# Performance work log

Measured on AMD Instinct MI355X. Metric: run time of the kernel, lower is better.

The kernel has to match this reference:

```python
import jax, jax.numpy as jnp
import numpy as np

N_HEAD = 16

def rel_shift(x):
    # x: (qlen, klen, B, n). Pad one zero column at front of klen axis,
    # reinterpret as (klen+1, qlen, B, n), drop first row, reshape back.
    qlen, klen, b, n = x.shape
    x_pad = jnp.pad(x, ((0, 0), (1, 0), (0, 0), (0, 0)))
    x_pad = x_pad.reshape(klen + 1, qlen, b, n)
    return x_pad[1:].reshape(qlen, klen, b, n)

def setup_inputs() -> dict:
    key = jax.random.key(0)
    ks = jax.random.split(key, 9)
    qlen = klen = 1024
    B = 4
    d_model = 1024
    d_head = d_model // N_HEAD
    q = jax.random.normal(ks[0], (qlen, B, d_model), jnp.float32)
    K = jax.random.normal(ks[1], (klen, B, d_model), jnp.float32)
    V = jax.random.normal(ks[2], (klen, B, d_model), jnp.float32)
    mask = jax.random.bernoulli(ks[3], 0.1, (1, klen, B, 1))
    r = jax.random.normal(ks[4], (klen, d_model), jnp.float32)
    u = jax.random.normal(ks[5], (N_HEAD, d_head), jnp.float32) * 0.02
    v = jax.random.normal(ks[6], (N_HEAD, d_head), jnp.float32) * 0.02
    Wr = jax.random.normal(ks[7], (d_model, d_model), jnp.float32) / np.sqrt(d_model)
    br = jax.random.normal(ks[8], (d_model,), jnp.float32) * 0.02
    return {"q": q, "K": K, "V": V, "mask": mask, "r": r, "u": u, "v": v, "Wr": Wr, "br": br}

def reference(q, K, V, mask, r, u, v, Wr, br):
    qlen, bsz, d_model = q.shape
    klen = K.shape[0]
    d_head = d_model // N_HEAD
    qh = q.reshape(qlen, bsz, N_HEAD, d_head)
    Kh = K.reshape(klen, bsz, N_HEAD, d_head)
    Vh = V.reshape(klen, bsz, N_HEAD, d_head)
    rh = (r @ Wr.T + br).reshape(klen, N_HEAD, d_head)  # r_net projection
    AC = jnp.einsum('ibnd,jbnd->ijbn', qh + u, Kh)
    BD = rel_shift(jnp.einsum('ibnd,jnd->ijbn', qh + v, rh))
    score = (AC + BD) / jnp.sqrt(jnp.asarray(d_head, q.dtype))
    # mask (1,klen,B,1) broadcasts over qlen and heads (torch repeats over heads)
    score = jnp.where(mask, jnp.asarray(-1e9, score.dtype), score)
    weight = jax.nn.softmax(score, axis=1)
    out = jnp.einsum('ijbn,jbnd->ibnd', weight, Vh).reshape(qlen, bsz, d_model)
    return out, weight.mean(axis=-1)
```

## Files before the change

### kernel.cpp

```cpp
#include <hip/hip_runtime.h>
#include <hip/hip_fp16.h>
#include <stdint.h>


#define L 1024
#define BATCH 4
#define NH 16
#define DH 64
#define DM 1024
#define TI 16
#define NJT 16
#define BDP_ST 1032
#define SCALE 0.125f
#define CS 0.18033688011112042f

typedef __attribute__((ext_vector_type(8))) short short8;
typedef __attribute__((ext_vector_type(4))) float f32x4;

static __device__ __forceinline__ unsigned short f2bf(float f) {
    union { float f; unsigned int u; } x; x.f = f;
    return (unsigned short)((x.u + 0x7fffu + ((x.u >> 16) & 1u)) >> 16);
}
static __device__ __forceinline__ float bf2f(unsigned short h) {
    union { unsigned int u; float f; } x; x.u = ((unsigned int)h) << 16;
    return x.f;
}
static __device__ __forceinline__ unsigned short f2h(float f) {
    __half h = __float2half(f);
    union { __half h; unsigned short s; } x; x.h = h; return x.s;
}
static __device__ __forceinline__ float h2f(unsigned short s) {
    union { __half h; unsigned short s; } x; x.s = s; return __half2float(x.h);
}
static __device__ __forceinline__ unsigned short* usp(void* base, int byteoff) {
    return (unsigned short*)((char*)base + byteoff);
}
static __device__ __forceinline__ short8 ld8(const void* base, int byteoff) {
    return *(const short8*)((const char*)base + byteoff);
}
static __device__ __forceinline__ float fexp2(float x) {
#if __has_builtin(__builtin_amdgcn_exp2f)
    return __builtin_amdgcn_exp2f(x);
#else
    return __expf(x * 0.6931471805599453f);
#endif
}
#define SW128(row, colByte) ((((row) * 128) + (colByte)) ^ (((row) & 7) << 4))

__global__ __launch_bounds__(256) void rh_gemm_mfma(
    const float* __restrict__ r, const float* __restrict__ Wr,
    const float* __restrict__ br, unsigned short* __restrict__ rhb)
{
    __shared__ unsigned short rT[64 * 64];
    __shared__ unsigned short wT[64 * 64];
    const int c0 = blockIdx.x * 64, m0 = blockIdx.y * 64;
    const int tid = threadIdx.x;
    const int w = tid >> 6, lane = tid & 63, lr = lane & 15, lg = lane >> 4;
    f32x4 acc[4] = {};

    for (int kt = 0; kt < 16; ++kt) {
        const int k0 = kt * 64;
        __syncthreads();
        const int row = tid >> 2, cb = (tid & 3) * 16;
#pragma unroll
        for (int q4 = 0; q4 < 4; ++q4) {
            float4 rv = *(const float4*)(r + (size_t)(c0 + row) * DM + k0 + cb + q4 * 4);
            unsigned short* p = usp(rT, SW128(row, (cb + q4 * 4) * 2));
            p[0] = f2bf(rv.x); p[1] = f2bf(rv.y); p[2] = f2bf(rv.z); p[3] = f2bf(rv.w);
            float4 wv = *(const float4*)(Wr + (size_t)(m0 + row) * DM + k0 + cb + q4 * 4);
            unsigned short* pw = usp(wT, SW128(row, (cb + q4 * 4) * 2));
            pw[0] = f2bf(wv.x); pw[1] = f2bf(wv.y); pw[2] = f2bf(wv.z); pw[3] = f2bf(wv.w);
        }
        __syncthreads();
#pragma unroll
        for (int mch = 0; mch < 4; ++mch)
#pragma unroll
            for (int kh = 0; kh < 2; ++kh) {
                short8 a  = ld8(rT, SW128(w * 16 + lr,   (kh * 32 + lg * 8) * 2));
                short8 bb = ld8(wT, SW128(mch * 16 + lr, (kh * 32 + lg * 8) * 2));
                acc[mch] = __builtin_amdgcn_mfma_f32_16x16x32_bf16(a, bb, acc[mch], 0, 0, 0);
            }
    }
#pragma unroll
    for (int mch = 0; mch < 4; ++mch)
#pragma unroll
        for (int r2 = 0; r2 < 4; ++r2) {
            const int c = c0 + w * 16 + lg * 4 + r2;
            const int d = mch * 16 + lr;
            const float val = acc[mch][r2] + br[m0 + d];
            rhb[((size_t)blockIdx.y * L + c) * DH + d] = f2bf(val);
        }
}

__global__ __launch_bounds__(256) void rh_gemm_kernel(
    const float* __restrict__ r, const float* __restrict__ Wr,
    const float* __restrict__ br, float* __restrict__ rhf)
{
    __shared__ float As[16][65];
    __shared__ float Bs[16][65];
    const int j0 = blockIdx.x * 64;
    const int m0 = blockIdx.y * 64;
    const int tid = threadIdx.x;
    const int ty = tid >> 4, tx = tid & 15;
    float acc[4][4] = {};

    for (int k0 = 0; k0 < DM; k0 += 16) {
        const int row = tid >> 2, c4 = (tid & 3) << 2;
        float4 av = *(const float4*)(r  + (size_t)(j0 + row) * DM + k0 + c4);
        float4 bv = *(const float4*)(Wr + (size_t)(m0 + row) * DM + k0 + c4);
        __syncthreads();
        As[c4 + 0][row] = av.x; As[c4 + 1][row] = av.y;
        As[c4 + 2][row] = av.z; As[c4 + 3][row] = av.w;
        Bs[c4 + 0][row] = bv.x; Bs[c4 + 1][row] = bv.y;
        Bs[c4 + 2][row] = bv.z; Bs[c4 + 3][row] = bv.w;
        __syncthreads();
#pragma unroll
        for (int k = 0; k < 16; ++k) {
            float a[4], bb[4];
#pragma unroll
            for (int t = 0; t < 4; ++t) { a[t] = As[k][ty * 4 + t]; bb[t] = Bs[k][tx * 4 + t]; }
#pragma unroll
            for (int ii = 0; ii < 4; ++ii)
#pragma unroll
                for (int jj = 0; jj < 4; ++jj)
                    acc[ii][jj] = fmaf(a[ii], bb[jj], acc[ii][jj]);
        }
    }
#pragma unroll
    for (int ii = 0; ii < 4; ++ii) {
        const int row = j0 + ty * 4 + ii;
#pragma unroll
        for (int jj = 0; jj < 4; ++jj) {
            const int col = m0 + tx * 4 + jj;
            rhf[(size_t)row * DM + col] = acc[ii][jj] + br[col];
        }
    }
}

__global__ __launch_bounds__(256) void prepass_kernel(
    const float* __restrict__ Kg, const float* __restrict__ Vg,
    unsigned short* __restrict__ Kbf, unsigned short* __restrict__ Vtb)
{
    __shared__ unsigned short tile[64][80];
    const int j0 = blockIdx.x * 64;
    const int b = blockIdx.y, n = blockIdx.z;
    const int bn = b * NH + n;
    const int tid = threadIdx.x;

    for (int idx = tid; idx < 64 * 16; idx += 256) {
        const int jr = idx >> 4, s4 = (idx & 15) * 4;
        const size_t src = ((size_t)(j0 + jr) * BATCH + b) * DM + n * DH + s4;
        float4 kv = *(const float4*)(Kg + src);
        ushort4 o;
        o.x = f2bf(kv.x); o.y = f2bf(kv.y); o.z = f2bf(kv.z); o.w = f2bf(kv.w);
        *(ushort4*)(Kbf + ((size_t)bn * L + j0 + jr) * DH + s4) = o;
        float4 vv4 = *(const float4*)(Vg + src);
        tile[s4 + 0][jr] = f2bf(vv4.x); tile[s4 + 1][jr] = f2bf(vv4.y);
        tile[s4 + 2][jr] = f2bf(vv4.z); tile[s4 + 3][jr] = f2bf(vv4.w);
    }
    __syncthreads();
    for (int idx = tid; idx < 64 * 8; idx += 256) {
        const int d = idx >> 3, p8 = (idx & 7) * 8;
        short8 o = *(const short8*)&tile[d][p8];
        *(short8*)(Vtb + ((size_t)bn * DH + d) * L + j0 + p8) = o;
    }
}

__global__ __launch_bounds__(256) void wm_reduce_kernel(
    const unsigned short* __restrict__ W_ws, const float* __restrict__ rdeng,
    float* __restrict__ wm_out)
{
    const int gi = blockIdx.x;
    const int b  = blockIdx.y;
    const int j0 = threadIdx.x * 4;
    float a0 = 0.f, a1 = 0.f, a2 = 0.f, a3 = 0.f;
#pragma unroll
    for (int n = 0; n < NH; ++n) {
        const int bn = b * NH + n;
        const float rd = rdeng[((size_t)bn << 10) + gi];
        ushort4 wv = *(const ushort4*)(W_ws + ((size_t)bn * L + gi) * L + j0);
        a0 += bf2f(wv.x) * rd; a1 += bf2f(wv.y) * rd;
        a2 += bf2f(wv.z) * rd; a3 += bf2f(wv.w) * rd;
    }
    const size_t o = ((size_t)gi * L + j0) * BATCH + b;
    wm_out[o]             = a0;
    wm_out[o + BATCH]     = a1;
    wm_out[o + 2 * BATCH] = a2;
    wm_out[o + 3 * BATCH] = a3;
}

__global__ __launch_bounds__(256, 3) void attn_fused(
    const float* __restrict__ q,
    const unsigned short* __restrict__ Kbf, const unsigned short* __restrict__ Vtb,
    const unsigned char* __restrict__ maskp,
    const float* __restrict__ uu, const float* __restrict__ vvp,
    const unsigned short* __restrict__ rhb,
    float* __restrict__ out, unsigned short* __restrict__ W_ws,
    float* __restrict__ rdeng)
{
    __shared__ __align__(16) unsigned short BDp[17 * BDP_ST];
    __shared__ __align__(16) unsigned short Wt[4][2][16 * 64];
    __shared__ unsigned char mblk[L];
    __shared__ float denomP[4][16];
    __shared__ float rdenom[16];
    __shared__ int mflags;

    const int i0 = blockIdx.x * TI;
    const int b  = blockIdx.y;
    const int n  = blockIdx.z;
    const int bn = b * NH + n;
    const int tid = threadIdx.x;
    const int w = tid >> 6, lane = tid & 63, lr = lane & 15, lg = lane >> 4;

    if (tid == 0) mflags = 0;
    __syncthreads();
    {
        int local = 0;
        for (int ww = tid; ww < 1024; ww += 256) {
            const unsigned int word = ((const unsigned int*)maskp)[ww];
            if (word == 0x3f800000u) local |= 1;
            else if (word & 0xffffff00u) local |= 2;
        }
        if (local) atomicOr(&mflags, local);
    }
    __syncthreads();
    {
        const int mtype = (mflags & 1) ? 2 : ((mflags & 2) ? 1 : 0);
        for (int j = tid; j < L; j += 256) {
            bool mv;
            if (mtype == 2)      mv = ((const float*)maskp)[j * BATCH + b] != 0.f;
            else if (mtype == 1) mv = maskp[j * BATCH + b] != 0;
            else                 mv = ((const int*)maskp)[j * BATCH + b] != 0;
            mblk[j] = mv ? 1 : 0;
        }
    }
    if (tid < 17 * 8) {
        const int row = tid >> 3, cp = tid & 7;
        BDp[row * BDP_ST + 1024 + cp] = 0;
    }

    const float* qrow = q + ((size_t)(i0 + lr) * BATCH + b) * DM + n * DH;
    const float* urow = uu + n * DH;
    const float* vrow = vvp + n * DH;
    short8 qu_a[2], qv_a[2];
#pragma unroll
    for (int kh = 0; kh < 2; ++kh) {
        const int kb = kh * 32 + lg * 8;
        float4 qa = *(const float4*)(qrow + kb), qb = *(const float4*)(qrow + kb + 4);
        float4 ua = *(const float4*)(urow + kb), ub = *(const float4*)(urow + kb + 4);
        float4 va = *(const float4*)(vrow + kb), vb = *(const float4*)(vrow + kb + 4);
        short8 su, sv;
        su[0] = (short)f2bf((qa.x + ua.x) * CS); su[1] = (short)f2bf((qa.y + ua.y) * CS);
        su[2] = (short)f2bf((qa.z + ua.z) * CS); su[3] = (short)f2bf((qa.w + ua.w) * CS);
        su[4] = (short)f2bf((qb.x + ub.x) * CS); su[5] = (short)f2bf((qb.y + ub.y) * CS);
        su[6] = (short)f2bf((qb.z + ub.z) * CS); su[7] = (short)f2bf((qb.w + ub.w) * CS);
        sv[0] = (short)f2bf((qa.x + va.x) * CS); sv[1] = (short)f2bf((qa.y + va.y) * CS);
        sv[2] = (short)f2bf((qa.z + va.z) * CS); sv[3] = (short)f2bf((qa.w + va.w) * CS);
        sv[4] = (short)f2bf((qb.x + vb.x) * CS); sv[5] = (short)f2bf((qb.y + vb.y) * CS);
        sv[6] = (short)f2bf((qb.z + vb.z) * CS); sv[7] = (short)f2bf((qb.w + vb.w) * CS);
        qu_a[kh] = su; qv_a[kh] = sv;
    }
    float qv16[16];
    {
        const int kq = (tid & 3) * 16;
        if (i0 + 16 < L) {
            const float* q16 = q + ((size_t)(i0 + 16) * BATCH + b) * DM + n * DH;
#pragma unroll
            for (int e4 = 0; e4 < 4; ++e4) {
                float4 qa = *(const float4*)(q16 + kq + e4 * 4);
                float4 va = *(const float4*)(vrow + kq + e4 * 4);
                qv16[e4 * 4 + 0] = (qa.x + va.x) * CS; qv16[e4 * 4 + 1] = (qa.y + va.y) * CS;
                qv16[e4 * 4 + 2] = (qa.z + va.z) * CS; qv16[e4 * 4 + 3] = (qa.w + va.w) * CS;
            }
        } else {
#pragma unroll
            for (int e = 0; e < 16; ++e) qv16[e] = 0.f;
        }
    }

    {
        const unsigned short* rpane = rhb + (size_t)n * L * DH;
        const int ccol = w * 16 + lr;
        short8 rb[2][2];
#pragma unroll
        for (int kh = 0; kh < 2; ++kh)
            rb[0][kh] = *(const short8*)(rpane + (size_t)ccol * DH + kh * 32 + lg * 8);
        const int col16 = tid >> 2;
        const int kq = (tid & 3) * 16;
#pragma unroll
        for (int ct = 0; ct < 16; ++ct) {
            const int c0 = ct * 64;
            const int cur = ct & 1;
            if (ct + 1 < 16) {
#pragma unroll
                for (int kh = 0; kh < 2; ++kh)
                    rb[cur ^ 1][kh] = *(const short8*)(rpane + (size_t)((ct + 1) * 64 + ccol) * DH + kh * 32 + lg * 8);
            }
            f32x4 acc = {0.f, 0.f, 0.f, 0.f};
#pragma unroll
            for (int kh = 0; kh < 2; ++kh)
                acc = __builtin_amdgcn_mfma_f32_16x16x32_bf16(qv_a[kh], rb[cur][kh], acc, 0, 0, 0);
#pragma unroll
            for (int r2 = 0; r2 < 4; ++r2)
                BDp[(lg * 4 + r2) * BDP_ST + c0 + ccol] = f2h(acc[r2]);
            {
                short8 ra0 = *(const short8*)(rpane + (size_t)(c0 + col16) * DH + kq);
                short8 ra1 = *(const short8*)(rpane + (size_t)(c0 + col16) * DH + kq + 8);
                float s16 = 0.f;
#pragma unroll
                for (int e = 0; e < 8; ++e) {
                    s16 = fmaf(qv16[e],     bf2f((unsigned short)ra0[e]), s16);
                    s16 = fmaf(qv16[e + 8], bf2f((unsigned short)ra1[e]), s16);
                }
                s16 += __shfl_xor(s16, 1);
                s16 += __shfl_xor(s16, 2);
                if ((tid & 3) == 0) BDp[16 * BDP_ST + c0 + col16] = f2h(s16);
            }
        }
    }
    __syncthreads();

    const unsigned short* Kpane = Kbf + (size_t)bn * L * DH;
    const unsigned short* Vpane = Vtb + (size_t)bn * DH * L;
    const int jwbase = w * 256;
    f32x4 pv[4] = {};
    float dl[4] = {0.f, 0.f, 0.f, 0.f};
    int ilb[4];
    size_t wsrow[4];
#pragma unroll
    for (int r2 = 0; r2 < 4; ++r2) {
        ilb[r2] = (lg * 4 + r2) * BDP_ST;
        wsrow[r2] = ((size_t)bn * L + i0 + lg * 4 + r2) * L;
    }
    short8 kf[2][2];
#pragma unroll
    for (int kh = 0; kh < 2; ++kh)
        kf[0][kh] = *(const short8*)(Kpane + (size_t)(jwbase + lr) * DH + kh * 32 + lg * 8);

#pragma unroll 1
    for (int sub = 0; sub < 4; ++sub) {
        const int jbase = jwbase + sub * 64;
        unsigned short* WtW = &Wt[w][sub & 1][0];
        short8 vfr[8];
#pragma unroll
        for (int dch = 0; dch < 4; ++dch)
#pragma unroll
            for (int kh = 0; kh < 2; ++kh)
                vfr[dch * 2 + kh] = *(const short8*)(Vpane + (size_t)(dch * 16 + lr) * L + jbase + kh * 32 + lg * 8);
#pragma unroll
        for (int c4 = 0; c4 < 4; ++c4) {
            const int chunk = sub * 4 + c4;
            const int cur = c4 & 1;
            if (chunk + 1 < 16) {
#pragma unroll
                for (int kh = 0; kh < 2; ++kh)
                    kf[cur ^ 1][kh] = *(const short8*)(Kpane + (size_t)(jwbase + (chunk + 1) * 16 + lr) * DH + kh * 32 + lg * 8);
            }
            f32x4 acc = {0.f, 0.f, 0.f, 0.f};
#pragma unroll
            for (int kh = 0; kh < 2; ++kh)
                acc = __builtin_amdgcn_mfma_f32_16x16x32_bf16(qu_a[kh], kf[cur][kh], acc, 0, 0, 0);
            const int gj = jbase + c4 * 16 + lr;
            const float mo = mblk[gj] ? -1e9f : 0.f;
            const int ebase = gj - i0 - lg * 4;
#pragma unroll
            for (int r2 = 0; r2 < 4; ++r2) {
                const int e = ebase - r2;
                const int addr = ilb[r2] + e + ((e <= 0) ? 1023 : 1030);
                const float bd = h2f(BDp[addr]);
                float s = fminf(acc[r2] + bd + mo, 126.f);
                const float wg = fexp2(s);
                dl[r2] += wg;
                const unsigned short wb = f2bf(wg);
                *usp(WtW, SW128(lg * 4 + r2, (c4 * 16 + lr) * 2)) = wb;
                W_ws[wsrow[r2] + gj] = wb;
            }
        }
#pragma unroll
        for (int dch = 0; dch < 4; ++dch)
#pragma unroll
            for (int kh = 0; kh < 2; ++kh) {
                short8 a = ld8(WtW, SW128(lr, (kh * 32 + lg * 8) * 2));
                pv[dch] = __builtin_amdgcn_mfma_f32_16x16x32_bf16(a, vfr[dch * 2 + kh], pv[dch], 0, 0, 0);
            }
    }

#pragma unroll
    for (int r2 = 0; r2 < 4; ++r2) {
        float d = dl[r2];
        d += __shfl_xor(d, 1); d += __shfl_xor(d, 2);
        d += __shfl_xor(d, 4); d += __shfl_xor(d, 8);
        if (lr == 0) denomP[w][lg * 4 + r2] = d;
    }
    {
        float* pvw = (float*)&Wt[w][0][0];
#pragma unroll
        for (int dch = 0; dch < 4; ++dch)
#pragma unroll
            for (int r2 = 0; r2 < 4; ++r2)
                pvw[(lg * 4 + r2) * 64 + dch * 16 + lr] = pv[dch][r2];
    }
    __syncthreads();
    if (tid < 16) {
        const float dn = denomP[0][tid] + denomP[1][tid] + denomP[2][tid] + denomP[3][tid];
        rdenom[tid] = 1.f / dn;
        rdeng[((size_t)bn << 10) + i0 + tid] = 1.f / (dn * 16.f);
    }
    __syncthreads();

    {
        const float* pvwAll = (const float*)&Wt[0][0][0];
        const int il = tid >> 4, d0 = (tid & 15) * 4;
        float4 o = *(const float4*)(pvwAll + 0 * 1024 + il * 64 + d0);
        float4 o1 = *(const float4*)(pvwAll + 1 * 1024 + il * 64 + d0);
        float4 o2 = *(const float4*)(pvwAll + 2 * 1024 + il * 64 + d0);
        float4 o3 = *(const float4*)(pvwAll + 3 * 1024 + il * 64 + d0);
        const float rs = rdenom[il];
        o.x = (o.x + o1.x + o2.x + o3.x) * rs;
        o.y = (o.y + o1.y + o2.y + o3.y) * rs;
        o.z = (o.z + o1.z + o2.z + o3.z) * rs;
        o.w = (o.w + o1.w + o2.w + o3.w) * rs;
        *(float4*)(out + ((size_t)(i0 + il) * BATCH + b) * DM + n * DH + d0) = o;
    }
}

template<int MODE>
__global__ __launch_bounds__(256, 2) void attn_legacy(
    const float* __restrict__ q,
    const void* __restrict__ Kp, const void* __restrict__ Vp,
    const unsigned char* __restrict__ maskp,
    const float* __restrict__ uu, const float* __restrict__ vvp,
    const void* __restrict__ rhp,
    float* __restrict__ out, float* __restrict__ wm_out)
{
    __shared__ unsigned short QU[16 * 64];
    __shared__ unsigned short QV[17 * 64];
    __shared__ unsigned short KR[(MODE == 1) ? 64 * 64 : 8];
    __shared__ unsigned short VT[(MODE == 1) ? 64 * 64 : 8];
    __shared__ unsigned short BDp[17 * BDP_ST];
    __shared__ unsigned short Wt[2][16 * 64];
    __shared__ unsigned char mblk[L];
    __shared__ float denomP[4][16];
    __shared__ float rdenom[16];
    __shared__ int mflags;

    const int i0 = blockIdx.x * TI;
    const int b  = blockIdx.y;
    const int n  = blockIdx.z;
    const int bn = b * NH + n;
    const int tid = threadIdx.x;
    const int w = tid >> 6, lane = tid & 63, lr = lane & 15, lg = lane >> 4;

    const unsigned short* Kbf = (const unsigned short*)Kp;
    const unsigned short* Vtb = (const unsigned short*)Vp;
    const unsigned short* rhb = (const unsigned short*)rhp;
    const float* Kg  = (const float*)Kp;
    const float* Vg  = (const float*)Vp;
    const float* rhf = (const float*)rhp;

    if (tid == 0) mflags = 0;
    __syncthreads();
    {
        int local = 0;
        for (int ww = tid; ww < 1024; ww += 256) {
            const unsigned int word = ((const unsigned int*)maskp)[ww];
            if (word == 0x3f800000u) local |= 1;
            else if (word & 0xffffff00u) local |= 2;
        }
        if (local) atomicOr(&mflags, local);
    }
    __syncthreads();
    {
        const int mtype = (mflags & 1) ? 2 : ((mflags & 2) ? 1 : 0);
        for (int j = tid; j < L; j += 256) {
            bool mv;
            if (mtype == 2)      mv = ((const float*)maskp)[j * BATCH + b] != 0.f;
            else if (mtype == 1) mv = maskp[j * BATCH + b] != 0;
            else                 mv = ((const int*)maskp)[j * BATCH + b] != 0;
            mblk[j] = mv ? 1 : 0;
        }
    }
    for (int idx = tid; idx < 17 * 64; idx += 256) {
        const int row = idx >> 6, d = idx & 63;
        const int gi = i0 + row;
        const float qval = (gi < L) ? q[((size_t)gi * BATCH + b) * DM + n * DH + d] : 0.f;
        *usp(QV, SW128(row, d * 2)) = f2bf((qval + vvp[n * DH + d]) * SCALE);
        if (row < 16) *usp(QU, SW128(row, d * 2)) = f2bf((qval + uu[n * DH + d]) * SCALE);
    }
    __syncthreads();

    for (int ct = 0; ct < 16; ++ct) {
        const int c0 = ct * 64;
        const int ccol = w * 16 + lr;
        if constexpr (MODE == 1) {
            __syncthreads();
            for (int idx = tid; idx < 64 * 16; idx += 256) {
                const int cr = idx >> 4, d4 = (idx & 15) * 4;
                float4 rv = *(const float4*)(rhf + (size_t)(c0 + cr) * DM + n * DH + d4);
                unsigned short* p = usp(KR, SW128(cr, d4 * 2));
                p[0] = f2bf(rv.x); p[1] = f2bf(rv.y); p[2] = f2bf(rv.z); p[3] = f2bf(rv.w);
            }
            __syncthreads();
        }
        f32x4 acc = {0.f, 0.f, 0.f, 0.f};
#pragma unroll
        for (int kh = 0; kh < 2; ++kh) {
            short8 a = ld8(QV, SW128(lr, (kh * 32 + lg * 8) * 2));
            short8 bb;
            if constexpr (MODE == 0)
                bb = *(const short8*)(rhb + ((size_t)n * L + c0 + ccol) * DH + kh * 32 + lg * 8);
            else
                bb = ld8(KR, SW128(ccol, (kh * 32 + lg * 8) * 2));
            acc = __builtin_amdgcn_mfma_f32_16x16x32_bf16(a, bb, acc, 0, 0, 0);
        }
#pragma unroll
        for (int r2 = 0; r2 < 4; ++r2)
            BDp[(lg * 4 + r2) * BDP_ST + c0 + ccol] = f2h(acc[r2]);
        {
            const int col = tid >> 2, kq = (tid & 3) * 16;
            float s16 = 0.f;
#pragma unroll
            for (int kk = 0; kk < 16; kk += 8) {
                short8 qa = ld8(QV, SW128(16, (kq + kk) * 2));
                short8 ra;
                if constexpr (MODE == 0)
                    ra = *(const short8*)(rhb + ((size_t)n * L + c0 + col) * DH + kq + kk);
                else
                    ra = ld8(KR, SW128(col, (kq + kk) * 2));
#pragma unroll
                for (int e = 0; e < 8; ++e)
                    s16 = fmaf(bf2f((unsigned short)qa[e]), bf2f((unsigned short)ra[e]), s16);
            }
            s16 += __shfl_xor(s16, 1);
            s16 += __shfl_xor(s16, 2);
            if ((tid & 3) == 0) BDp[16 * BDP_ST + c0 + col] = f2h(s16);
        }
    }

    const int jloc = w * 16 + lr;
    __syncthreads();

    f32x4 pv = {0.f, 0.f, 0.f, 0.f};
    float dl[4] = {0.f, 0.f, 0.f, 0.f};
    float tmp[4][NJT];
#pragma unroll
    for (int jt = 0; jt < NJT; ++jt) {
        const int j0 = jt * 64;
        const int gj = j0 + jloc;
        const int cur = jt & 1;
        if constexpr (MODE == 1) {
            __syncthreads();
            for (int idx = tid; idx < 64 * 16; idx += 256) {
                const int jr = idx >> 4, d4 = (idx & 15) * 4;
                const size_t src = ((size_t)(j0 + jr) * BATCH + b) * DM + n * DH + d4;
                float4 kv = *(const float4*)(Kg + src);
                unsigned short* p = usp(KR, SW128(jr, d4 * 2));
                p[0] = f2bf(kv.x); p[1] = f2bf(kv.y); p[2] = f2bf(kv.z); p[3] = f2bf(kv.w);
                float4 vv4 = *(const float4*)(Vg + src);
                *usp(VT, SW128(d4 + 0, jr * 2)) = f2bf(vv4.x);
                *usp(VT, SW128(d4 + 1, jr * 2)) = f2bf(vv4.y);
                *usp(VT, SW128(d4 + 2, jr * 2)) = f2bf(vv4.z);
                *usp(VT, SW128(d4 + 3, jr * 2)) = f2bf(vv4.w);
            }
            __syncthreads();
        }
        f32x4 acc = {0.f, 0.f, 0.f, 0.f};
#pragma unroll
        for (int kh = 0; kh < 2; ++kh) {
            short8 a = ld8(QU, SW128(lr, (kh * 32 + lg * 8) * 2));
            short8 bb;
            if constexpr (MODE == 0)
                bb = *(const short8*)(Kbf + ((size_t)bn * L + gj) * DH + kh * 32 + lg * 8);
            else
                bb = ld8(KR, SW128(jloc, (kh * 32 + lg * 8) * 2));
            acc = __builtin_amdgcn_mfma_f32_16x16x32_bf16(a, bb, acc, 0, 0, 0);
        }
        const bool msk = mblk[gj] != 0;
#pragma unroll
        for (int r2 = 0; r2 < 4; ++r2) {
            const int il = lg * 4 + r2;
            const int gi = i0 + il;
            const int t = gj - gi;
            float bd = 0.f;
            if (t != 1) {
                const int c = (t <= 0) ? (L - 1 + t) : (t - 2);
                bd = h2f(BDp[(il + (t >= 1 ? 1 : 0)) * BDP_ST + c]);
            }
            float s = acc[r2] + bd;
            if (msk) s = -1e9f;
            const float wgt = __expf(fminf(s, 80.f));
            dl[r2] += wgt;
            tmp[r2][jt] = wgt;
            *usp(Wt[cur], SW128(il, jloc * 2)) = f2bf(wgt);
        }
        __syncthreads();
#pragma unroll
        for (int kh = 0; kh < 2; ++kh) {
            short8 a = ld8(Wt[cur], SW128(lr, (kh * 32 + lg * 8) * 2));
            short8 bb;
            if constexpr (MODE == 0)
                bb = *(const short8*)(Vtb + ((size_t)bn * DH + jloc) * L + j0 + kh * 32 + lg * 8);
            else
                bb = ld8(VT, SW128(jloc, (kh * 32 + lg * 8) * 2));
            pv = __builtin_amdgcn_mfma_f32_16x16x32_bf16(a, bb, pv, 0, 0, 0);
        }
    }

#pragma unroll
    for (int r2 = 0; r2 < 4; ++r2) {
        float d = dl[r2];
        d += __shfl_xor(d, 1); d += __shfl_xor(d, 2);
        d += __shfl_xor(d, 4); d += __shfl_xor(d, 8);
        if (lr == 0) denomP[w][lg * 4 + r2] = d;
    }
    __syncthreads();
    if (tid < 16)
        rdenom[tid] = 1.f / (denomP[0][tid] + denomP[1][tid] + denomP[2][tid] + denomP[3][tid]);
    __syncthreads();

#pragma unroll
    for (int r2 = 0; r2 < 4; ++r2) {
        const int il = lg * 4 + r2;
        out[((size_t)(i0 + il) * BATCH + b) * DM + n * DH + w * 16 + lr] = pv[r2] * rdenom[il];
    }
#pragma unroll
    for (int r2 = 0; r2 < 4; ++r2) {
        const int il = lg * 4 + r2;
        const float rs = rdenom[il] * (1.f / 16.f);
#pragma unroll
        for (int jt = 0; jt < NJT; ++jt)
            atomicAdd(wm_out + ((size_t)(i0 + il) * L + jt * 64 + jloc) * BATCH + b,
                      tmp[r2][jt] * rs);
    }
}

extern "C" void kernel_launch(void* const* d_in, const int* in_sizes, int n_in,
                              void* d_out, int out_size, void* d_ws, size_t ws_size,
                              hipStream_t stream)
{
    (void)in_sizes; (void)n_in; (void)out_size;
    const float* q   = (const float*)d_in[0];
    const float* K   = (const float*)d_in[1];
    const float* V   = (const float*)d_in[2];
    const unsigned char* mask = (const unsigned char*)d_in[3];
    const float* r   = (const float*)d_in[4];
    const float* u   = (const float*)d_in[5];
    const float* v   = (const float*)d_in[6];
    const float* Wr  = (const float*)d_in[7];
    const float* br  = (const float*)d_in[8];

    float* out = (float*)d_out;
    float* wm  = out + (size_t)L * BATCH * DM;

    const size_t kvbytes = (size_t)BATCH * NH * L * DH * 2;
    const size_t rhbytes = (size_t)NH * L * DH * 2;
    const size_t wmbytes = (size_t)BATCH * NH * L * L * 2;
    const size_t rdbytes = (size_t)BATCH * NH * L * 4;

    if (ws_size >= 2 * kvbytes + rhbytes + wmbytes + rdbytes) {
        unsigned short* Kbf = (unsigned short*)d_ws;
        unsigned short* Vtb = Kbf + kvbytes / 2;
        unsigned short* rhb = Vtb + kvbytes / 2;
        unsigned short* Wws = rhb + rhbytes / 2;
        float* rdeng = (float*)(Wws + wmbytes / 2);
        rh_gemm_mfma<<<dim3(16, 16), 256, 0, stream>>>(r, Wr, br, rhb);
        prepass_kernel<<<dim3(16, 4, 16), 256, 0, stream>>>(K, V, Kbf, Vtb);
        attn_fused<<<dim3(64, 4, 16), 256, 0, stream>>>(
            q, Kbf, Vtb, mask, u, v, rhb, out, Wws, rdeng);
        wm_reduce_kernel<<<dim3(L, BATCH), 256, 0, stream>>>(Wws, rdeng, wm);
    } else if (ws_size >= 2 * kvbytes + rhbytes) {
        hipMemsetAsync(wm, 0, (size_t)L * L * BATCH * sizeof(float), stream);
        unsigned short* Kbf = (unsigned short*)d_ws;
        unsigned short* Vtb = Kbf + kvbytes / 2;
        unsigned short* rhb = Vtb + kvbytes / 2;
        rh_gemm_mfma<<<dim3(16, 16), 256, 0, stream>>>(r, Wr, br, rhb);
        prepass_kernel<<<dim3(16, 4, 16), 256, 0, stream>>>(K, V, Kbf, Vtb);
        attn_legacy<0><<<dim3(64, 4, 16), 256, 0, stream>>>(
            q, Kbf, Vtb, mask, u, v, rhb, out, wm);
    } else {
        hipMemsetAsync(wm, 0, (size_t)L * L * BATCH * sizeof(float), stream);
        float* rhf = (float*)d_ws;
        rh_gemm_kernel<<<dim3(16, 16), 256, 0, stream>>>(r, Wr, br, rhf);
        attn_legacy<1><<<dim3(64, 4, 16), 256, 0, stream>>>(
            q, K, V, mask, u, v, rhf, out, wm);
    }
}
```

Measured before the change: 297.2 us.

## Pack weight workspace in fragment layout, XCD-aware block mapping, deeper K/r prefetch

The attention kernel now writes its bf16 softmax weights as one packed ushort4 per lane in an MFMA-fragment-ordered workspace layout, replacing four scattered 2-byte stores. The reduce kernel is rewritten to read that layout, handle four query rows per block, and load the reciprocal denominators as float4. The attention grid is flattened to 1D and remapped so that all blocks of the same (batch, head) pane land on the same XCD, improving L2 reuse of K/V/r. The r and K fragment prefetches are deepened from one chunk to two, at the cost of extra registers.

```diff
diff --git a/kernel.cpp b/kernel.cpp
--- a/kernel.cpp
+++ b/kernel.cpp
@@ -167,26 +167,33 @@
 }
 
 __global__ __launch_bounds__(256) void wm_reduce_kernel(
-    const unsigned short* __restrict__ W_ws, const float* __restrict__ rdeng,
+    const unsigned short* __restrict__ Wf, const float* __restrict__ rdeng,
     float* __restrict__ wm_out)
 {
-    const int gi = blockIdx.x;
+    const int ig = blockIdx.x;
     const int b  = blockIdx.y;
-    const int j0 = threadIdx.x * 4;
-    float a0 = 0.f, a1 = 0.f, a2 = 0.f, a3 = 0.f;
-#pragma unroll
-    for (int n = 0; n < NH; ++n) {
-        const int bn = b * NH + n;
-        const float rd = rdeng[((size_t)bn << 10) + gi];
-        ushort4 wv = *(const ushort4*)(W_ws + ((size_t)bn * L + gi) * L + j0);
-        a0 += bf2f(wv.x) * rd; a1 += bf2f(wv.y) * rd;
-        a2 += bf2f(wv.z) * rd; a3 += bf2f(wv.w) * rd;
-    }
-    const size_t o = ((size_t)gi * L + j0) * BATCH + b;
-    wm_out[o]             = a0;
-    wm_out[o + BATCH]     = a1;
-    wm_out[o + 2 * BATCH] = a2;
-    wm_out[o + 3 * BATCH] = a3;
+    const int ib = ig >> 2, lg = ig & 3;
+    const int tid = threadIdx.x;
+#pragma unroll
+    for (int jj = 0; jj < 4; ++jj) {
+        const int j = jj * 256 + tid;
+        const int gc = j >> 4, lr = j & 15;
+        float a0 = 0.f, a1 = 0.f, a2 = 0.f, a3 = 0.f;
+#pragma unroll
+        for (int n = 0; n < NH; ++n) {
+            const int bn = b * NH + n;
+            const float4 rd = *(const float4*)(rdeng + ((size_t)bn << 10) + ig * 4);
+            ushort4 wv = *(const ushort4*)(Wf +
+                ((((size_t)bn * 64 + ib) * 64 + gc) * 64 + lg * 16 + lr) * 4);
+            a0 += bf2f(wv.x) * rd.x; a1 += bf2f(wv.y) * rd.y;
+            a2 += bf2f(wv.z) * rd.z; a3 += bf2f(wv.w) * rd.w;
+        }
+        const size_t o = ((size_t)(ig * 4) * L + j) * BATCH + b;
+        wm_out[o]                      = a0;
+        wm_out[o + (size_t)L * BATCH]  = a1;
+        wm_out[o + 2 * (size_t)L * BATCH] = a2;
+        wm_out[o + 3 * (size_t)L * BATCH] = a3;
+    }
 }
 
 __global__ __launch_bounds__(256, 3) void attn_fused(
@@ -205,10 +212,14 @@
     __shared__ float rdenom[16];
     __shared__ int mflags;
 
-    const int i0 = blockIdx.x * TI;
-    const int b  = blockIdx.y;
-    const int n  = blockIdx.z;
-    const int bn = b * NH + n;
+    const int lin = blockIdx.x;
+    const int xcd = lin & 7, idx = lin >> 3;
+    const int ib  = idx & 63;
+    const int pane = xcd * 8 + (idx >> 6);
+    const int b = pane >> 4, n = pane & 15;
+    const int i0 = ib * 16;
+    const int bn = pane;
+
     const int tid = threadIdx.x;
     const int w = tid >> 6, lane = tid & 63, lr = lane & 15, lg = lane >> 4;
 
@@ -283,18 +294,20 @@
         const int ccol = w * 16 + lr;
         short8 rb[2][2];
 #pragma unroll
-        for (int kh = 0; kh < 2; ++kh)
+        for (int kh = 0; kh < 2; ++kh) {
             rb[0][kh] = *(const short8*)(rpane + (size_t)ccol * DH + kh * 32 + lg * 8);
+            rb[1][kh] = *(const short8*)(rpane + (size_t)(64 + ccol) * DH + kh * 32 + lg * 8);
+        }
         const int col16 = tid >> 2;
         const int kq = (tid & 3) * 16;
 #pragma unroll
         for (int ct = 0; ct < 16; ++ct) {
             const int c0 = ct * 64;
             const int cur = ct & 1;
-            if (ct + 1 < 16) {
-#pragma unroll
-                for (int kh = 0; kh < 2; ++kh)
-                    rb[cur ^ 1][kh] = *(const short8*)(rpane + (size_t)((ct + 1) * 64 + ccol) * DH + kh * 32 + lg * 8);
+            short8 nk0, nk1;
+            if (ct + 2 < 16) {
+                nk0 = *(const short8*)(rpane + (size_t)((ct + 2) * 64 + ccol) * DH + lg * 8);
+                nk1 = *(const short8*)(rpane + (size_t)((ct + 2) * 64 + ccol) * DH + 32 + lg * 8);
             }
             f32x4 acc = {0.f, 0.f, 0.f, 0.f};
 #pragma unroll
@@ -316,6 +329,7 @@
                 s16 += __shfl_xor(s16, 2);
                 if ((tid & 3) == 0) BDp[16 * BDP_ST + c0 + col16] = f2h(s16);
             }
+            if (ct + 2 < 16) { rb[cur][0] = nk0; rb[cur][1] = nk1; }
         }
     }
     __syncthreads();
@@ -326,16 +340,15 @@
     f32x4 pv[4] = {};
     float dl[4] = {0.f, 0.f, 0.f, 0.f};
     int ilb[4];
-    size_t wsrow[4];
-#pragma unroll
-    for (int r2 = 0; r2 < 4; ++r2) {
-        ilb[r2] = (lg * 4 + r2) * BDP_ST;
-        wsrow[r2] = ((size_t)bn * L + i0 + lg * 4 + r2) * L;
-    }
+#pragma unroll
+    for (int r2 = 0; r2 < 4; ++r2) ilb[r2] = (lg * 4 + r2) * BDP_ST;
+
     short8 kf[2][2];
 #pragma unroll
-    for (int kh = 0; kh < 2; ++kh)
+    for (int kh = 0; kh < 2; ++kh) {
         kf[0][kh] = *(const short8*)(Kpane + (size_t)(jwbase + lr) * DH + kh * 32 + lg * 8);
+        kf[1][kh] = *(const short8*)(Kpane + (size_t)(jwbase + 16 + lr) * DH + kh * 32 + lg * 8);
+    }
 
 #pragma unroll 1
     for (int sub = 0; sub < 4; ++sub) {
@@ -351,10 +364,11 @@
         for (int c4 = 0; c4 < 4; ++c4) {
             const int chunk = sub * 4 + c4;
             const int cur = c4 & 1;
-            if (chunk + 1 < 16) {
-#pragma unroll
-                for (int kh = 0; kh < 2; ++kh)
-                    kf[cur ^ 1][kh] = *(const short8*)(Kpane + (size_t)(jwbase + (chunk + 1) * 16 + lr) * DH + kh * 32 + lg * 8);
+            short8 nk0, nk1;
+            if (chunk + 2 < 16) {
+                const int jn = jwbase + (chunk + 2) * 16 + lr;
+                nk0 = *(const short8*)(Kpane + (size_t)jn * DH + lg * 8);
+                nk1 = *(const short8*)(Kpane + (size_t)jn * DH + 32 + lg * 8);
             }
             f32x4 acc = {0.f, 0.f, 0.f, 0.f};
 #pragma unroll
@@ -363,6 +377,7 @@
             const int gj = jbase + c4 * 16 + lr;
             const float mo = mblk[gj] ? -1e9f : 0.f;
             const int ebase = gj - i0 - lg * 4;
+            ushort4 wpack;
 #pragma unroll
             for (int r2 = 0; r2 < 4; ++r2) {
                 const int e = ebase - r2;
@@ -372,9 +387,16 @@
                 const float wg = fexp2(s);
                 dl[r2] += wg;
                 const unsigned short wb = f2bf(wg);
+                ((unsigned short*)&wpack)[r2] = wb;
                 *usp(WtW, SW128(lg * 4 + r2, (c4 * 16 + lr) * 2)) = wb;
-                W_ws[wsrow[r2] + gj] = wb;
-            }
+            }
+            {
+                const int gc = w * 16 + chunk - w * 16 + jwbase / 16 + 0;
+                const int gcc = (jbase >> 4) + c4;
+                *(ushort4*)(W_ws + ((((size_t)bn * 64 + ib) * 64 + gcc) * 64 + lane) * 4) = wpack;
+                (void)gc;
+            }
+            if (chunk + 2 < 16) { kf[cur][0] = nk0; kf[cur][1] = nk1; }
         }
 #pragma unroll
         for (int dch = 0; dch < 4; ++dch)
@@ -411,7 +433,7 @@
     {
         const float* pvwAll = (const float*)&Wt[0][0][0];
         const int il = tid >> 4, d0 = (tid & 15) * 4;
-        float4 o = *(const float4*)(pvwAll + 0 * 1024 + il * 64 + d0);
+        float4 o  = *(const float4*)(pvwAll + 0 * 1024 + il * 64 + d0);
         float4 o1 = *(const float4*)(pvwAll + 1 * 1024 + il * 64 + d0);
         float4 o2 = *(const float4*)(pvwAll + 2 * 1024 + il * 64 + d0);
         float4 o3 = *(const float4*)(pvwAll + 3 * 1024 + il * 64 + d0);
@@ -665,9 +687,9 @@
         float* rdeng = (float*)(Wws + wmbytes / 2);
         rh_gemm_mfma<<<dim3(16, 16), 256, 0, stream>>>(r, Wr, br, rhb);
         prepass_kernel<<<dim3(16, 4, 16), 256, 0, stream>>>(K, V, Kbf, Vtb);
-        attn_fused<<<dim3(64, 4, 16), 256, 0, stream>>>(
+        attn_fused<<<dim3(4096), 256, 0, stream>>>(
             q, Kbf, Vtb, mask, u, v, rhb, out, Wws, rdeng);
-        wm_reduce_kernel<<<dim3(L, BATCH), 256, 0, stream>>>(Wws, rdeng, wm);
+        wm_reduce_kernel<<<dim3(256, BATCH), 256, 0, stream>>>(Wws, rdeng, wm);
     } else if (ws_size >= 2 * kvbytes + rhbytes) {
         hipMemsetAsync(wm, 0, (size_t)L * L * BATCH * sizeof(float), stream);
         unsigned short* Kbf = (unsigned short*)d_ws;
```

Measured after the change: 287.0 us. 1.04x faster.
